# Kernel tuning notes

Hardware: AMD Instinct MI355X
Metric: run time of the kernel (lower is better)

## Reference

```python
import jax, jax.numpy as jnp
import numpy as np

EMBED = 512
HEADS = 8
DIM_HEAD = 64          # embed_dim // 8
LANDMARKS = 256        # embed_dim // 2
PINV_ITERS = 6
RES_K = 33             # nystrom residual_conv_kernel default
SCALE = DIM_HEAD ** -0.5


def layer_norm(x, g, b, eps=1e-5):
    mu = x.mean(-1, keepdims=True)
    var = ((x - mu) ** 2).mean(-1, keepdims=True)
    return (x - mu) / jnp.sqrt(var + eps) * g + b


def moore_penrose_pinv(x, iters=PINV_ITERS):
    # iterative Moore-Penrose pseudo-inverse (lucidrains nystrom-attention)
    ax = jnp.abs(x)
    z = jnp.swapaxes(x, -1, -2) / (ax.sum(-1).max() * ax.sum(-2).max())
    I = jnp.eye(x.shape[-1], dtype=x.dtype)
    for _ in range(iters):
        xz = x @ z
        z = 0.25 * z @ (13. * I - xz @ (15. * I - xz @ (7. * I - xz)))
    return z


def nystrom_attention(x, w_qkv, w_out, b_out, res_k):
    b, n, _ = x.shape
    m = LANDMARKS
    pad = (m - n % m) % m
    xp = jnp.pad(x, ((0, 0), (pad, 0), (0, 0)))  # left-pad like F.pad(..., padding, 0)
    np_ = n + pad
    qkv = (xp @ w_qkv).reshape(b, np_, 3, HEADS, DIM_HEAD)
    q = qkv[:, :, 0].transpose(0, 2, 1, 3) * SCALE   # [b,h,np,dh]
    k = qkv[:, :, 1].transpose(0, 2, 1, 3)
    v = qkv[:, :, 2].transpose(0, 2, 1, 3)
    l = np_ // m
    q_l = q.reshape(b, HEADS, m, l, DIM_HEAD).mean(3)  # [b,h,m,dh]
    k_l = k.reshape(b, HEADS, m, l, DIM_HEAD).mean(3)
    attn1 = jax.nn.softmax(jnp.einsum('bhid,bhjd->bhij', q, k_l), -1)    # [b,h,np,m]
    attn2 = jax.nn.softmax(jnp.einsum('bhid,bhjd->bhij', q_l, k_l), -1)  # [b,h,m,m]
    attn3 = jax.nn.softmax(jnp.einsum('bhid,bhjd->bhij', q_l, k), -1)    # [b,h,m,np]
    out = (attn1 @ moore_penrose_pinv(attn2)) @ (attn3 @ v)              # [b,h,np,dh]
    # depthwise residual conv over the sequence dim, per head (shared across dh)
    v_c = v.transpose(0, 3, 1, 2).reshape(b * DIM_HEAD, HEADS, np_)
    res = jax.lax.conv_general_dilated(
        v_c, res_k[:, None, :], (1,), [(RES_K // 2, RES_K // 2)],
        dimension_numbers=('NCH', 'OIH', 'NCH'), feature_group_count=HEADS)
    out = out + res.reshape(b, DIM_HEAD, HEADS, np_).transpose(0, 2, 3, 1)
    out = out.transpose(0, 2, 1, 3).reshape(b, np_, HEADS * DIM_HEAD)
    out = out @ w_out + b_out
    return out[:, -n:]  # drop left padding


def dwconv2d(x, w, b, k):
    # x: [B,C,H,W], w: [C,1,k,k] depthwise
    y = jax.lax.conv_general_dilated(
        x, w, (1, 1), [(k // 2, k // 2)] * 2,
        dimension_numbers=('NCHW', 'OIHW', 'NCHW'), feature_group_count=x.shape[1])
    return y + b[None, :, None, None]


def ppeg(x, H, W, w7, b7, w5, b5, w3, b3):
    B, _, C = x.shape
    cls_tok, feat = x[:, :1], x[:, 1:]
    f = feat.transpose(0, 2, 1).reshape(B, C, H, W)
    y = f + dwconv2d(f, w7, b7, 7) + dwconv2d(f, w5, b5, 5) + dwconv2d(f, w3, b3, 3)
    y = y.reshape(B, C, H * W).transpose(0, 2, 1)
    return jnp.concatenate([cls_tok, y], axis=1)


def reference(h, w_fc1, b_fc1, cls_token,
              ln1_g, ln1_b, qkv1_w, out1_w, out1_b, res1_k,
              conv7_w, conv7_b, conv5_w, conv5_b, conv3_w, conv3_b,
              ln2_g, ln2_b, qkv2_w, out2_w, out2_b, res2_k,
              lnf_g, lnf_b):
    h = jax.nn.relu(h @ w_fc1 + b_fc1)                 # [B,N,512]
    B, N, C = h.shape
    _H = int(np.ceil(np.sqrt(N)))
    add = _H * _H - N
    h = jnp.concatenate([h, h[:, :add]], axis=1)       # square padding
    h = jnp.concatenate([jnp.broadcast_to(cls_token, (B, 1, C)), h], axis=1)
    h = h + nystrom_attention(layer_norm(h, ln1_g, ln1_b), qkv1_w, out1_w, out1_b, res1_k)
    h = ppeg(h, _H, _H, conv7_w, conv7_b, conv5_w, conv5_b, conv3_w, conv3_b)
    h = h + nystrom_attention(layer_norm(h, ln2_g, ln2_b), qkv2_w, out2_w, out2_b, res2_k)
    return layer_norm(h, lnf_g, lnf_b)[:, 0]           # [B,512]


def setup_inputs() -> dict:
    key = jax.random.key(0)
    ks = jax.random.split(key, 24)
    B, N, IN_DIM = 2, 4096, 1024
    w = lambda k, shape, s=0.02: jax.random.normal(k, shape, jnp.float32) * s
    z = lambda shape: jnp.zeros(shape, jnp.float32)
    o = lambda shape: jnp.ones(shape, jnp.float32)
    return {
        'h': jax.random.normal(ks[0], (B, N, IN_DIM), jnp.float32),
        'w_fc1': w(ks[1], (IN_DIM, EMBED)), 'b_fc1': z((EMBED,)),
        'cls_token': w(ks[2], (1, 1, EMBED)),
        'ln1_g': o((EMBED,)), 'ln1_b': z((EMBED,)),
        'qkv1_w': w(ks[3], (EMBED, 3 * HEADS * DIM_HEAD)),
        'out1_w': w(ks[4], (HEADS * DIM_HEAD, EMBED)), 'out1_b': z((EMBED,)),
        'res1_k': w(ks[5], (HEADS, RES_K), 0.1),
        'conv7_w': w(ks[6], (EMBED, 1, 7, 7), 0.05), 'conv7_b': z((EMBED,)),
        'conv5_w': w(ks[7], (EMBED, 1, 5, 5), 0.05), 'conv5_b': z((EMBED,)),
        'conv3_w': w(ks[8], (EMBED, 1, 3, 3), 0.05), 'conv3_b': z((EMBED,)),
        'ln2_g': o((EMBED,)), 'ln2_b': z((EMBED,)),
        'qkv2_w': w(ks[9], (EMBED, 3 * HEADS * DIM_HEAD)),
        'out2_w': w(ks[10], (HEADS * DIM_HEAD, EMBED)), 'out2_b': z((EMBED,)),
        'res2_k': w(ks[11], (HEADS, RES_K), 0.1),
        'lnf_g': o((EMBED,)), 'lnf_b': z((EMBED,)),
    }
```

## Files before the change

kernel.cpp:

```cpp
#include <hip/hip_runtime.h>
#include <hip/hip_bf16.h>

#define HEADS 8
#define DH 64
#define EMB 512
#define NP 4352
#define NTOK 4097
#define PADF 255
#define LM 256
#define SCALE 0.125f

typedef __attribute__((ext_vector_type(8))) short bf8;
typedef __attribute__((ext_vector_type(4))) float f4;
typedef __attribute__((ext_vector_type(8))) unsigned short us8;
typedef __attribute__((ext_vector_type(4))) unsigned short us4;
typedef unsigned short u16;

__device__ __forceinline__ u16 f2b(float f){
  union { float f; unsigned u; } x; x.f = f;
  unsigned r = x.u + 0x7fffu + ((x.u>>16)&1u);
  return (u16)(r>>16);
}
__device__ __forceinline__ float b2f(u16 h){
  union { unsigned u; float f; } x; x.u = ((unsigned)h)<<16;
  return x.f;
}

__device__ __forceinline__ void gload_lds(const u16* g, u16* l){
  __builtin_amdgcn_global_load_lds((const __attribute__((address_space(1))) void*)g,
                                   (__attribute__((address_space(3))) void*)l, 16, 0, 0);
}

template<int MODE>
__global__ __launch_bounds__(256)
void k_g128(const u16* __restrict__ A, const u16* __restrict__ B,
            float* __restrict__ C, u16* __restrict__ C16,
            int K, int lda, int ldb, int ldc,
            long sAb, long sAh, long sBb, long sBh, long sCb, long sCh, int nh,
            float alpha, const float* __restrict__ bias, int relu, int rowoff,
            int nx, int ksplit)
{
  int z = blockIdx.z;
  const u16* Ab = A + (long)(z/nh)*sAb + (long)(z%nh)*sAh;
  const u16* Bb = B + (long)(z/nh)*sBb + (long)(z%nh)*sBh;
  long cb = (long)(z/nh)*sCb + (long)(z%nh)*sCh;
  int bx = blockIdx.x % nx, kc = blockIdx.x / nx;
  int m0 = blockIdx.y*128, n0 = bx*128;
  int klen = K/ksplit, kbeg = kc*klen, nch = klen/32;
  __shared__ u16 As[2][4096];
  __shared__ u16 Bs[2][4096];
  int tid=threadIdx.x, w=tid>>6, lane=tid&63, q=lane>>4, lr=lane&15;
  int wrow=(w>>1)*64, wcol=(w&1)*64;
  int srow = tid>>2, scol = (tid&3)*8;
  const u16* ga  = Ab + (long)(m0+srow)*lda + kbeg + scol;
  const u16* ga2 = Ab + (long)(m0+64+srow)*lda + kbeg + scol;
  const u16* gb  = Bb + (long)(n0+srow)*ldb + kbeg + scol;
  const u16* gb2 = Bb + (long)(n0+64+srow)*ldb + kbeg + scol;
  int lo = srow*32 + scol;
  f4 acc[4][4] = {};
  auto stage = [&](int r, int c){
    gload_lds(ga  + c*32, &As[r][lo]);
    gload_lds(ga2 + c*32, &As[r][2048+lo]);
    gload_lds(gb  + c*32, &Bs[r][lo]);
    gload_lds(gb2 + c*32, &Bs[r][2048+lo]);
  };
  auto compute = [&](int r){
    bf8 af[4], bfr[4];
    #pragma unroll
    for(int rr=0;rr<4;rr++) af[rr]  = *(const bf8*)&As[r][(wrow + rr*16 + lr)*32 + q*8];
    #pragma unroll
    for(int t=0;t<4;t++) bfr[t] = *(const bf8*)&Bs[r][(wcol + t*16 + lr)*32 + q*8];
    #pragma unroll
    for(int rr=0;rr<4;rr++)
      #pragma unroll
      for(int t=0;t<4;t++)
        acc[rr][t] = __builtin_amdgcn_mfma_f32_16x16x32_bf16(af[rr], bfr[t], acc[rr][t], 0,0,0);
  };
  stage(0,0);
  __syncthreads();
  for(int c=1;c<nch;c++){
    stage(c&1, c);
    compute((c-1)&1);
    __syncthreads();
  }
  compute((nch-1)&1);
  #pragma unroll
  for(int r=0;r<4;r++){
    #pragma unroll
    for(int t=0;t<4;t++){
      #pragma unroll
      for(int e=0;e<4;e++){
        int gm = m0 + wrow + r*16 + q*4 + e;
        int gn = n0 + wcol + t*16 + lr;
        float v = acc[r][t][e]*alpha;
        if(MODE==4){
          if(bias && kc==0) v += bias[gn];
          if(gm>=rowoff) atomicAdd(&C[cb + (long)(gm-rowoff)*ldc + gn], v);
        } else {
          if(bias) v += bias[gn];
          if(relu) v = fmaxf(v,0.f);
          if(MODE==0) C[cb + (long)gm*ldc + gn] = v;
          else if(MODE==2) C16[cb + (long)gm*ldc + gn] = f2b(v);
          else { if(gm>=rowoff) C[cb + (long)(gm-rowoff)*ldc + gn] += v; }
        }
      }
    }
  }
}

template<int MODE>
__global__ __launch_bounds__(256)
void k_g64(const u16* __restrict__ A, const u16* __restrict__ B,
           float* __restrict__ C, u16* __restrict__ C16,
           int K, int lda, int ldb, int ldc,
           long sAb, long sAh, long sBb, long sBh, long sCb, long sCh, int nh,
           float alpha, const float* __restrict__ bias, int rowoff, int moff,
           int nx, int ksplit)
{
  int z = blockIdx.z;
  const u16* Ab = A + (long)(z/nh)*sAb + (long)(z%nh)*sAh;
  const u16* Bb = B + (long)(z/nh)*sBb + (long)(z%nh)*sBh;
  long cb = (long)(z/nh)*sCb + (long)(z%nh)*sCh;
  int bx = blockIdx.x % nx, kc = blockIdx.x / nx;
  int m0 = blockIdx.y*64 + moff, n0 = bx*64;
  int klen = K/ksplit, kbeg = kc*klen, nch = klen/32;
  __shared__ u16 As[2][2048];
  __shared__ u16 Bs[2][2048];
  int tid=threadIdx.x, w=tid>>6, lane=tid&63, q=lane>>4, lr=lane&15;
  int srow = tid>>2, scol = (tid&3)*8;
  const u16* ga = Ab + (long)(m0+srow)*lda + kbeg + scol;
  const u16* gb = Bb + (long)(n0+srow)*ldb + kbeg + scol;
  int lo = srow*32 + scol;
  f4 acc[4] = {};
  auto stage = [&](int r, int c){
    gload_lds(ga + c*32, &As[r][lo]);
    gload_lds(gb + c*32, &Bs[r][lo]);
  };
  auto compute = [&](int r){
    bf8 af = *(const bf8*)&As[r][(w*16 + lr)*32 + q*8];
    #pragma unroll
    for(int t=0;t<4;t++){
      bf8 bfr = *(const bf8*)&Bs[r][(t*16 + lr)*32 + q*8];
      acc[t] = __builtin_amdgcn_mfma_f32_16x16x32_bf16(af, bfr, acc[t], 0,0,0);
    }
  };
  stage(0,0);
  __syncthreads();
  for(int c=1;c<nch;c++){
    stage(c&1, c);
    compute((c-1)&1);
    __syncthreads();
  }
  compute((nch-1)&1);
  #pragma unroll
  for(int t=0;t<4;t++){
    #pragma unroll
    for(int e=0;e<4;e++){
      int gm = m0 + w*16 + q*4 + e;
      int gn = n0 + t*16 + lr;
      float v = acc[t][e]*alpha;
      if(MODE==0) C[cb + (long)gm*ldc + gn] = v;
      else if(MODE==2) C16[cb + (long)gm*ldc + gn] = f2b(v);
      else if(MODE==3) atomicAdd(&C[cb + (long)gm*ldc + gn], v);
      else if(MODE==5){
        v += bias[gn];
        if(gm>=rowoff) C[cb + (long)(gm-rowoff)*ldc + gn] += v;
      }
    }
  }
}

__global__ __launch_bounds__(256)
void k_pg3(const u16* __restrict__ Ah, const u16* __restrict__ Al,
           const u16* __restrict__ Bh, const u16* __restrict__ Bl,
           u16* __restrict__ Oh, u16* __restrict__ Ol, float na, float nd,
           u16* __restrict__ TOh, u16* __restrict__ TOl, float ta, float td)
{
  long zo = (long)blockIdx.z*65536;
  int m0 = blockIdx.y*32, n0 = blockIdx.x*64;
  __shared__ u16 S[2][6144];
  int tid=threadIdx.x, w=tid>>6, lane=tid&63, q=lane>>4, lr=lane&15;
  int t2 = tid & 127;
  const u16* srcA = (tid<128 ? Ah : Al) + zo + (long)(m0 + (t2>>2))*256 + (t2&3)*8;
  const u16* srcBh = Bh + zo + (long)(n0 + (tid>>2))*256 + (tid&3)*8;
  const u16* srcBl = Bl + zo + (long)(n0 + (tid>>2))*256 + (tid&3)*8;
  f4 acc[2] = {};
  auto stage = [&](int r, int c){
    gload_lds(srcA  + c*32, &S[r][tid*8]);
    gload_lds(srcBh + c*32, &S[r][2048 + tid*8]);
    gload_lds(srcBl + c*32, &S[r][4096 + tid*8]);
  };
  int mrow = (w>>1)*16 + lr;
  auto compute = [&](int r){
    bf8 ah = *(const bf8*)&S[r][mrow*32 + q*8];
    bf8 al = *(const bf8*)&S[r][1024 + mrow*32 + q*8];
    #pragma unroll
    for(int t=0;t<2;t++){
      int nrow = (w&1)*32 + t*16 + lr;
      bf8 bh = *(const bf8*)&S[r][2048 + nrow*32 + q*8];
      bf8 bl = *(const bf8*)&S[r][4096 + nrow*32 + q*8];
      acc[t] = __builtin_amdgcn_mfma_f32_16x16x32_bf16(ah, bh, acc[t], 0,0,0);
      acc[t] = __builtin_amdgcn_mfma_f32_16x16x32_bf16(ah, bl, acc[t], 0,0,0);
      acc[t] = __builtin_amdgcn_mfma_f32_16x16x32_bf16(al, bh, acc[t], 0,0,0);
    }
  };
  stage(0,0);
  __syncthreads();
  #pragma unroll
  for(int c=1;c<8;c++){
    stage(c&1, c);
    compute((c-1)&1);
    __syncthreads();
  }
  compute(1);
  #pragma unroll
  for(int t=0;t<2;t++){
    int gn = n0 + (w&1)*32 + t*16 + lr;
    if(Oh){
      #pragma unroll
      for(int r=0;r<4;r++){
        int gm = m0 + (w>>1)*16 + q*4 + r;
        float v = na*acc[t][r] + ((gm==gn)?nd:0.f);
        u16 h = f2b(v);
        long o = zo + (long)gm*256 + gn;
        Oh[o] = h; Ol[o] = f2b(v - b2f(h));
      }
    }
    if(TOh){
      us4 th, tl;
      #pragma unroll
      for(int r=0;r<4;r++){
        int gm = m0 + (w>>1)*16 + q*4 + r;
        float v = ta*acc[t][r] + ((gm==gn)?td:0.f);
        u16 h = f2b(v);
        th[r] = h; tl[r] = f2b(v - b2f(h));
      }
      long o = zo + (long)gn*256 + (m0 + (w>>1)*16 + q*4);
      *(us4*)&TOh[o] = th; *(us4*)&TOl[o] = tl;
    }
  }
}

__global__ __launch_bounds__(256)
void k_pg3b(const u16* __restrict__ Zh, const u16* __restrict__ Zl,
            const u16* __restrict__ Ph, const u16* __restrict__ Pl,
            const u16* __restrict__ Bh, const u16* __restrict__ Bl,
            u16* __restrict__ Ozh, u16* __restrict__ Ozl,
            u16* __restrict__ Oyh, u16* __restrict__ Oyl,
            u16* __restrict__ Tyh, u16* __restrict__ Tyl)
{
  long zo = (long)blockIdx.z*65536;
  int ysel = blockIdx.y>>3;
  int m0 = (blockIdx.y&7)*32, n0 = blockIdx.x*64;
  const u16* Ah = ysel ? Ph : Zh;
  const u16* Al = ysel ? Pl : Zl;
  __shared__ u16 S[2][6144];
  int tid=threadIdx.x, w=tid>>6, lane=tid&63, q=lane>>4, lr=lane&15;
  int t2 = tid & 127;
  const u16* srcA = (tid<128 ? Ah : Al) + zo + (long)(m0 + (t2>>2))*256 + (t2&3)*8;
  const u16* srcBh = Bh + zo + (long)(n0 + (tid>>2))*256 + (tid&3)*8;
  const u16* srcBl = Bl + zo + (long)(n0 + (tid>>2))*256 + (tid&3)*8;
  f4 acc[2] = {};
  auto stage = [&](int r, int c){
    gload_lds(srcA  + c*32, &S[r][tid*8]);
    gload_lds(srcBh + c*32, &S[r][2048 + tid*8]);
    gload_lds(srcBl + c*32, &S[r][4096 + tid*8]);
  };
  int mrow = (w>>1)*16 + lr;
  auto compute = [&](int r){
    bf8 ah = *(const bf8*)&S[r][mrow*32 + q*8];
    bf8 al = *(const bf8*)&S[r][1024 + mrow*32 + q*8];
    #pragma unroll
    for(int t=0;t<2;t++){
      int nrow = (w&1)*32 + t*16 + lr;
      bf8 bh = *(const bf8*)&S[r][2048 + nrow*32 + q*8];
      bf8 bl = *(const bf8*)&S[r][4096 + nrow*32 + q*8];
      acc[t] = __builtin_amdgcn_mfma_f32_16x16x32_bf16(ah, bh, acc[t], 0,0,0);
      acc[t] = __builtin_amdgcn_mfma_f32_16x16x32_bf16(ah, bl, acc[t], 0,0,0);
      acc[t] = __builtin_amdgcn_mfma_f32_16x16x32_bf16(al, bh, acc[t], 0,0,0);
    }
  };
  stage(0,0);
  __syncthreads();
  #pragma unroll
  for(int c=1;c<8;c++){
    stage(c&1, c);
    compute((c-1)&1);
    __syncthreads();
  }
  compute(1);
  #pragma unroll
  for(int t=0;t<2;t++){
    int gn = n0 + (w&1)*32 + t*16 + lr;
    if(!ysel){
      #pragma unroll
      for(int r=0;r<4;r++){
        int gm = m0 + (w>>1)*16 + q*4 + r;
        float v = 0.25f*acc[t][r];
        u16 h = f2b(v);
        long o = zo + (long)gm*256 + gn;
        Ozh[o] = h; Ozl[o] = f2b(v - b2f(h));
      }
    } else {
      us4 th, tl;
      #pragma unroll
      for(int r=0;r<4;r++){
        int gm = m0 + (w>>1)*16 + q*4 + r;
        float v = 0.25f*acc[t][r];
        u16 h = f2b(v);
        long o = zo + (long)gm*256 + gn;
        Oyh[o] = h; Oyl[o] = f2b(v - b2f(h));
        float tv = -v + ((gm==gn)?7.f:0.f);
        u16 h2 = f2b(tv);
        th[r] = h2; tl[r] = f2b(tv - b2f(h2));
      }
      long o = zo + (long)gn*256 + (m0 + (w>>1)*16 + q*4);
      *(us4*)&Tyh[o] = th; *(us4*)&Tyl[o] = tl;
    }
  }
}

__global__ __launch_bounds__(256)
void k_att3(const u16* __restrict__ qkv16, const u16* __restrict__ ql,
            const u16* __restrict__ vT, float* __restrict__ partO,
            float* __restrict__ pm, float* __restrict__ pl)
{
  int kc = blockIdx.x, jt = blockIdx.y, z = blockIdx.z;
  int b = z>>3, h = z&7;
  __shared__ u16 SQ[64*64];
  __shared__ u16 SK[2][64*64];
  __shared__ u16 SV[2][64*64];
  __shared__ u16 SP[64*64];
  int tid=threadIdx.x, w=tid>>6, lane=tid&63, q=lane>>4, lr=lane&15;
  const u16* kb = qkv16 + (long)b*NP*1536 + 512 + h*64;
  const u16* vb = vT + (long)z*64*NP;
  int t00 = kc*256;
  {
    const u16* qb = ql + (long)z*16384 + jt*64*64;
    #pragma unroll
    for(int p=0;p<2;p++){
      int idx = tid + p*256; int row = idx>>3; int js = ((idx&7)^(row&7))<<3;
      gload_lds(qb + row*64 + js, &SQ[idx*8]);
    }
  }
  auto stageKV = [&](int r, int i){
    int t0 = t00 + i*64;
    #pragma unroll
    for(int p=0;p<2;p++){
      int idx = tid + p*256; int row = idx>>3; int js = ((idx&7)^(row&7))<<3;
      gload_lds(kb + (long)(t0+row)*1536 + js, &SK[r][idx*8]);
      gload_lds(vb + (long)row*NP + t0 + js, &SV[r][idx*8]);
    }
  };
  stageKV(0,0);
  __syncthreads();
  int ar = w*16+lr;
  bf8 af0 = *(const bf8*)&SQ[ar*64 + ((q^(ar&7))<<3)];
  bf8 af1 = *(const bf8*)&SQ[ar*64 + (((q|4)^(ar&7))<<3)];
  f4 o[4] = {};
  float m[4] = {-3e38f,-3e38f,-3e38f,-3e38f};
  float l[4] = {0.f,0.f,0.f,0.f};
  for(int i=0;i<4;i++){
    int cur = i&1;
    if(i<3) stageKV(cur^1, i+1);
    f4 s[4] = {};
    #pragma unroll
    for(int t=0;t<4;t++){
      int br = t*16+lr;
      bf8 b0 = *(const bf8*)&SK[cur][br*64 + ((q^(br&7))<<3)];
      bf8 b1 = *(const bf8*)&SK[cur][br*64 + (((q|4)^(br&7))<<3)];
      s[t] = __builtin_amdgcn_mfma_f32_16x16x32_bf16(af0, b0, s[t], 0,0,0);
      s[t] = __builtin_amdgcn_mfma_f32_16x16x32_bf16(af1, b1, s[t], 0,0,0);
    }
    float tm[4];
    #pragma unroll
    for(int e=0;e<4;e++) tm[e] = fmaxf(fmaxf(s[0][e],s[1][e]), fmaxf(s[2][e],s[3][e]));
    #pragma unroll
    for(int sh=1; sh<16; sh<<=1)
      #pragma unroll
      for(int e=0;e<4;e++) tm[e] = fmaxf(tm[e], __shfl_xor(tm[e], sh));
    float rs[4];
    #pragma unroll
    for(int e=0;e<4;e++){
      float mn = fmaxf(m[e], tm[e]);
      float sc = expf(m[e]-mn);
      m[e] = mn;
      l[e] *= sc;
      rs[e] = 0.f;
      o[0][e]*=sc; o[1][e]*=sc; o[2][e]*=sc; o[3][e]*=sc;
    }
    #pragma unroll
    for(int t=0;t<4;t++)
      #pragma unroll
      for(int e=0;e<4;e++){
        float p = expf(s[t][e]-m[e]);
        rs[e] += p;
        int prow = w*16+q*4+e, pcol = t*16+lr;
        SP[prow*64 + (((pcol>>3)^(prow&7))<<3) + (pcol&7)] = f2b(p);
      }
    #pragma unroll
    for(int sh=1; sh<16; sh<<=1)
      #pragma unroll
      for(int e=0;e<4;e++) rs[e] += __shfl_xor(rs[e], sh);
    #pragma unroll
    for(int e=0;e<4;e++) l[e] += rs[e];
    int pr = w*16+lr;
    #pragma unroll
    for(int ks=0;ks<2;ks++){
      bf8 pa = *(const bf8*)&SP[pr*64 + (((ks*4+q)^(pr&7))<<3)];
      #pragma unroll
      for(int t2=0;t2<4;t2++){
        int rr = t2*16+lr;
        bf8 vv = *(const bf8*)&SV[cur][rr*64 + (((ks*4+q)^(rr&7))<<3)];
        o[t2] = __builtin_amdgcn_mfma_f32_16x16x32_bf16(pa, vv, o[t2], 0,0,0);
      }
    }
    __syncthreads();
  }
  long pb = (long)(z*17+kc)*256 + jt*64 + w*16;
  #pragma unroll
  for(int e=0;e<4;e++){
    int jg = q*4+e;
    #pragma unroll
    for(int t2=0;t2<4;t2++)
      partO[(pb + jg)*64 + t2*16 + lr] = o[t2][e];
    if(lr==0){ pm[pb + jg] = m[e]; pl[pb + jg] = l[e]; }
  }
}

__global__ __launch_bounds__(128)
void k_mrg3(const float* __restrict__ partO, const float* __restrict__ pm,
            const float* __restrict__ pl, u16* __restrict__ avbT16)
{
  int jq = blockIdx.x, z = blockIdx.y, tid = threadIdx.x;
  int j0 = jq*16;
  __shared__ float wk[16][17];
  __shared__ u16 T[16][72];
  if(tid < 16){
    int j = j0 + tid;
    float mm[17];
    float M = -3e38f;
    #pragma unroll
    for(int kc=0;kc<17;kc++){ mm[kc]=pm[(z*17+kc)*256 + j]; M=fmaxf(M,mm[kc]); }
    float s = 0.f;
    #pragma unroll
    for(int kc=0;kc<17;kc++){ float e=expf(mm[kc]-M); wk[tid][kc]=e; s+=e*pl[(z*17+kc)*256 + j]; }
    float inv = 1.f/s;
    #pragma unroll
    for(int kc=0;kc<17;kc++) wk[tid][kc]*=inv;
  }
  __syncthreads();
  float acc[8];
  #pragma unroll
  for(int p=0;p<8;p++) acc[p]=0.f;
  for(int kc=0;kc<17;kc++){
    long base = ((long)(z*17+kc)*256 + j0)*64;
    #pragma unroll
    for(int p=0;p<8;p++){
      int idx = tid + p*128;
      acc[p] += wk[idx>>6][kc]*partO[base + idx];
    }
  }
  #pragma unroll
  for(int p=0;p<8;p++){ int idx = tid + p*128; T[idx>>6][idx&63] = f2b(acc[p]); }
  __syncthreads();
  int d = tid>>1, jh = (tid&1)*8;
  us8 vv;
  #pragma unroll
  for(int u=0;u<8;u++) vv[u] = T[jh+u][d];
  *(us8*)&avbT16[(long)(z*64+d)*256 + j0 + jh] = vv;
}

__global__ __launch_bounds__(256)
void k_att1(const u16* __restrict__ qkv16, const u16* __restrict__ kl,
            const u16* __restrict__ zavT, float* __restrict__ Qc)
{
  int z = blockIdx.y, b = z>>3, h = z&7;
  int m0 = blockIdx.x*64;
  __shared__ u16 SQ[64*64];
  __shared__ u16 SKL[256*64];
  __shared__ u16 SZV[64*256];
  int tid=threadIdx.x, w=tid>>6, lane=tid&63, q=lane>>4, lr=lane&15;
  {
    const u16* qb = qkv16 + (long)b*NP*1536 + h*64;
    #pragma unroll
    for(int p=0;p<2;p++){
      int idx = tid + p*256; int row = idx>>3; int js = ((idx&7)^(row&7))<<3;
      gload_lds(qb + (long)(m0+row)*1536 + js, &SQ[idx*8]);
    }
    const u16* kb = kl + (long)z*16384;
    #pragma unroll
    for(int p=0;p<8;p++){
      int idx = tid + p*256; int row = idx>>3; int js = ((idx&7)^(row&7))<<3;
      gload_lds(kb + row*64 + js, &SKL[idx*8]);
    }
    const u16* zb = zavT + (long)z*16384;
    #pragma unroll
    for(int p=0;p<8;p++){
      int idx = tid + p*256; int row = idx>>5; int cs = ((idx&31)^(row&7))<<3;
      gload_lds(zb + row*256 + cs, &SZV[idx*8]);
    }
  }
  __syncthreads();
  f4 acc[16] = {};
  {
    int ar = w*16+lr;
    bf8 af0 = *(const bf8*)&SQ[ar*64 + ((q^(ar&7))<<3)];
    bf8 af1 = *(const bf8*)&SQ[ar*64 + (((q|4)^(ar&7))<<3)];
    #pragma unroll
    for(int t=0;t<16;t++){
      int br = t*16+lr;
      bf8 b0 = *(const bf8*)&SKL[br*64 + ((q^(br&7))<<3)];
      bf8 b1 = *(const bf8*)&SKL[br*64 + (((q|4)^(br&7))<<3)];
      acc[t] = __builtin_amdgcn_mfma_f32_16x16x32_bf16(af0, b0, acc[t], 0,0,0);
      acc[t] = __builtin_amdgcn_mfma_f32_16x16x32_bf16(af1, b1, acc[t], 0,0,0);
    }
  }
  float mx[4] = {-1e30f,-1e30f,-1e30f,-1e30f};
  #pragma unroll
  for(int t=0;t<16;t++)
    #pragma unroll
    for(int e=0;e<4;e++) mx[e] = fmaxf(mx[e], acc[t][e]*SCALE);
  #pragma unroll
  for(int s=1;s<16;s<<=1)
    #pragma unroll
    for(int e=0;e<4;e++) mx[e] = fmaxf(mx[e], __shfl_xor(mx[e], s));
  float sm[4] = {0.f,0.f,0.f,0.f};
  #pragma unroll
  for(int t=0;t<16;t++)
    #pragma unroll
    for(int e=0;e<4;e++){ float p = expf(acc[t][e]*SCALE - mx[e]); acc[t][e]=p; sm[e]+=p; }
  #pragma unroll
  for(int s=1;s<16;s<<=1)
    #pragma unroll
    for(int e=0;e<4;e++) sm[e] += __shfl_xor(sm[e], s);
  float inv[4];
  #pragma unroll
  for(int e=0;e<4;e++) inv[e] = 1.f/sm[e];
  __syncthreads();
  u16* PS = SKL;
  #pragma unroll
  for(int t=0;t<16;t++)
    #pragma unroll
    for(int e=0;e<4;e++){
      int prow = w*16 + q*4 + e, pcol = t*16 + lr;
      PS[prow*256 + (((pcol>>3)^(prow&7))<<3) + (pcol&7)] = f2b(acc[t][e]*inv[e]);
    }
  __syncthreads();
  f4 acc2[4] = {};
  int pr = w*16+lr;
  #pragma unroll
  for(int ks=0;ks<8;ks++){
    bf8 af = *(const bf8*)&PS[pr*256 + (((ks*4+q)^(pr&7))<<3)];
    #pragma unroll
    for(int t=0;t<4;t++){
      int rr = t*16+lr;
      bf8 bf_ = *(const bf8*)&SZV[rr*256 + (((ks*4+q)^(rr&7))<<3)];
      acc2[t] = __builtin_amdgcn_mfma_f32_16x16x32_bf16(af, bf_, acc2[t], 0,0,0);
    }
  }
  #pragma unroll
  for(int t=0;t<4;t++)
    #pragma unroll
    for(int r=0;r<4;r++){
      int gm = m0 + w*16 + q*4 + r;
      int gd = t*16 + lr;
      Qc[((long)b*NP + gm)*512 + h*64 + gd] = acc2[t][r];
    }
}

__global__ __launch_bounds__(256)
void k_smw32(float* __restrict__ X){
  long row = (long)blockIdx.x*4 + (threadIdx.x>>6);
  int lane = threadIdx.x & 63;
  float* p = X + row*256;
  float4 v = *(float4*)&p[lane*4];
  float m = fmaxf(fmaxf(v.x,v.y),fmaxf(v.z,v.w));
  for(int s=32;s;s>>=1) m = fmaxf(m, __shfl_xor(m, s));
  float e0=expf(v.x-m), e1=expf(v.y-m), e2=expf(v.z-m), e3=expf(v.w-m);
  float sum = e0+e1+e2+e3;
  for(int s=32;s;s>>=1) sum += __shfl_xor(sum, s);
  float inv = 1.f/sum;
  float4 o = {e0*inv, e1*inv, e2*inv, e3*inv};
  *(float4*)&p[lane*4] = o;
}

__global__ void k_wT(const float* __restrict__ in, u16* __restrict__ out, int K, int N){
  int n0=blockIdx.x*32, k0=blockIdx.y*32, tid=threadIdx.x;
  __shared__ float T[32][33];
  int lr=tid&31, lc=tid>>5;
  #pragma unroll
  for(int p=0;p<4;p++) T[lc+8*p][lr] = in[(long)(k0+lc+8*p)*N + n0+lr];
  __syncthreads();
  #pragma unroll
  for(int p=0;p<4;p++) out[(long)(n0+lc+8*p)*K + k0+lr] = f2b(T[lr][lc+8*p]);
}

__global__ __launch_bounds__(256)
void k_vT(const u16* __restrict__ qkv16, u16* __restrict__ vT){
  int t0=blockIdx.x*64, h=blockIdx.y, b=blockIdx.z, tid=threadIdx.x;
  __shared__ u16 T[64][72];
  const u16* src = qkv16 + (long)b*NP*1536 + 1024 + h*64;
  for(int s=0;s<2;s++){
    int idx=tid+s*256; int row=idx>>3, c8=(idx&7)*8;
    *(us8*)&T[row][c8] = *(const us8*)&src[(long)(t0+row)*1536 + c8];
  }
  __syncthreads();
  u16* dst = vT + ((long)(b*8+h)*64)*NP;
  int d = tid>>2, j0=(tid&3)*16;
  us8 v0,v1;
  #pragma unroll
  for(int jj=0;jj<8;jj++){ v0[jj]=T[j0+jj][d]; v1[jj]=T[j0+8+jj][d]; }
  *(us8*)&dst[(long)d*NP + t0 + j0]     = v0;
  *(us8*)&dst[(long)d*NP + t0 + j0 + 8] = v1;
}

__global__ void k_cvt16(const float* __restrict__ in, u16* __restrict__ out, long n){
  long i = (long)blockIdx.x*256 + threadIdx.x;
  if(i<n) out[i] = f2b(in[i]);
}

__global__ void k_cls(const float* __restrict__ cls, float* __restrict__ seq){
  int b = blockIdx.x;
  seq[(long)b*NTOK*EMB + threadIdx.x] = cls[threadIdx.x];
}

__global__ void k_ln_pad(const float* __restrict__ seq, u16* __restrict__ xp,
                         const float* __restrict__ g, const float* __restrict__ bb){
  int b = blockIdx.y, i = blockIdx.x, tid = threadIdx.x;
  u16* out = xp + ((long)b*NP + i)*EMB;
  if(i < PADF){ out[tid]=0; out[tid+256]=0; return; }
  const float* x = seq + ((long)b*NTOK + (i-PADF))*EMB;
  float v0 = x[tid], v1 = x[tid+256];
  __shared__ float red[256];
  red[tid]=v0+v1; __syncthreads();
  for(int s=128;s>0;s>>=1){ if(tid<s) red[tid]+=red[tid+s]; __syncthreads(); }
  float mu = red[0]*(1.0f/512.0f); __syncthreads();
  float d0=v0-mu, d1=v1-mu;
  red[tid]=d0*d0+d1*d1; __syncthreads();
  for(int s=128;s>0;s>>=1){ if(tid<s) red[tid]+=red[tid+s]; __syncthreads(); }
  float rstd = rsqrtf(red[0]*(1.0f/512.0f) + 1e-5f);
  out[tid]     = f2b(d0*rstd*g[tid]     + bb[tid]);
  out[tid+256] = f2b(d1*rstd*g[tid+256] + bb[tid+256]);
}

__global__ void k_landmarks(const u16* __restrict__ qkv, u16* __restrict__ q_l, u16* __restrict__ k_l){
  int j = blockIdx.x*4 + (threadIdx.x>>6), h = blockIdx.y, b = blockIdx.z, d = threadIdx.x&63;
  const u16* base = qkv + (long)b*NP*1536 + h*64 + d;
  float sq=0.f, sk=0.f;
  for(int l=0;l<17;l++){
    long row = (long)(j*17+l)*1536;
    sq += b2f(base[row]);
    sk += b2f(base[row+512]);
  }
  long o = (((long)b*HEADS + h)*LM + j)*DH + d;
  q_l[o] = f2b(sq * (SCALE/17.0f));
  k_l[o] = f2b(sk * (1.0f/17.0f));
}

__global__ void k_pinv_norm(const float* __restrict__ A2, float* __restrict__ rmax, float* __restrict__ cmax){
  int z = blockIdx.x, tid = threadIdx.x;
  const float* X = A2 + (long)z*65536;
  float rs=0.f, cs=0.f;
  for(int j=0;j<256;j++){ rs += fabsf(X[tid*256+j]); cs += fabsf(X[j*256+tid]); }
  __shared__ float r1[256], r2[256];
  r1[tid]=rs; r2[tid]=cs; __syncthreads();
  for(int s=128;s>0;s>>=1){ if(tid<s){ r1[tid]=fmaxf(r1[tid],r1[tid+s]); r2[tid]=fmaxf(r2[tid],r2[tid+s]); } __syncthreads(); }
  if(tid==0){ rmax[z]=r1[0]; cmax[z]=r2[0]; }
}

__global__ void k_pair_init(const float* __restrict__ att2,
    const float* __restrict__ rmax, const float* __restrict__ cmax,
    u16* __restrict__ Xh, u16* __restrict__ Xl,
    u16* __restrict__ Zh, u16* __restrict__ Zl,
    u16* __restrict__ Zth, u16* __restrict__ Ztl)
{
  long zo = (long)blockIdx.z*65536;
  int i0 = blockIdx.y*64, j0 = blockIdx.x*64;
  float rm=0.f, cm=0.f;
  for(int t=0;t<16;t++){ rm=fmaxf(rm,rmax[t]); cm=fmaxf(cm,cmax[t]); }
  float inv = 1.0f/(rm*cm);
  __shared__ float T[64][68];
  int tid = threadIdx.x;
  int li = tid>>2, jc = (tid&3)*16;
  #pragma unroll
  for(int u=0;u<4;u++){
    float4 v = *(const float4*)&att2[zo + (long)(i0+li)*256 + j0 + jc + u*4];
    T[li][jc+u*4]=v.x; T[li][jc+u*4+1]=v.y; T[li][jc+u*4+2]=v.z; T[li][jc+u*4+3]=v.w;
    long o = zo + (long)(i0+li)*256 + j0 + jc + u*4;
    float vv[4] = {v.x,v.y,v.z,v.w};
    us4 xh, xl, zth, ztl;
    #pragma unroll
    for(int c=0;c<4;c++){
      u16 h = f2b(vv[c]); xh[c]=h; xl[c]=f2b(vv[c]-b2f(h));
      float zt = vv[c]*inv;
      u16 h2 = f2b(zt); zth[c]=h2; ztl[c]=f2b(zt-b2f(h2));
    }
    *(us4*)&Xh[o]=xh; *(us4*)&Xl[o]=xl; *(us4*)&Zth[o]=zth; *(us4*)&Ztl[o]=ztl;
  }
  __syncthreads();
  int lj = tid>>2, ic = (tid&3)*16;
  #pragma unroll
  for(int r=0;r<16;r++){
    float x = T[ic+r][lj]*inv;
    u16 h = f2b(x);
    long o = zo + (long)(j0+lj)*256 + i0 + ic + r;
    Zh[o]=h; Zl[o]=f2b(x-b2f(h));
  }
}

__global__ __launch_bounds__(256)
void k_rconv(const u16* __restrict__ qkv16, const float* __restrict__ resk,
             const float* __restrict__ Qin, u16* __restrict__ Qo16){
  int t0 = blockIdx.x*64, h = blockIdx.y, b = blockIdx.z;
  __shared__ float V[96*64];
  const u16* vb = qkv16 + (long)b*NP*1536 + 1024 + h*64;
  int tid = threadIdx.x;
  #pragma unroll
  for(int s=0;s<3;s++){
    int idx = tid + s*256;
    int row = idx>>3, c8 = (idx&7)*8;
    int p = t0 - 16 + row;
    if(p>=0 && p<NP){
      us8 v = *(const us8*)&vb[(long)p*1536 + c8];
      #pragma unroll
      for(int jj=0;jj<8;jj++) V[row*64+c8+jj] = b2f(v[jj]);
    } else {
      #pragma unroll
      for(int jj=0;jj<8;jj++) V[row*64+c8+jj] = 0.f;
    }
  }
  __syncthreads();
  int d = tid&63, lt = (tid>>6)*16;
  float acc[16] = {};
  #pragma unroll
  for(int s=0;s<48;s++){
    float val = V[(lt+s)*64 + d];
    #pragma unroll
    for(int j=0;j<16;j++){
      int tap = s - j;
      if(tap>=0 && tap<33) acc[j] += resk[h*33+tap]*val;
    }
  }
  #pragma unroll
  for(int j=0;j<16;j++){
    long idx = ((long)b*NP + t0 + lt + j)*EMB + h*64 + d;
    Qo16[idx] = f2b(Qin[idx] + acc[j]);
  }
}

__global__ __launch_bounds__(256)
void k_ppeg(const float* __restrict__ seq, float* __restrict__ out,
    const float* __restrict__ w7,const float* __restrict__ b7,
    const float* __restrict__ w5,const float* __restrict__ b5,
    const float* __restrict__ w3,const float* __restrict__ b3){
  int b = blockIdx.z, cg = blockIdx.y;
  int rp = blockIdx.x>>1, xs = blockIdx.x&1;
  int ch0 = cg*64;
  __shared__ float s7[64*49], s5[64*25], s3[64*9], sbias[64];
  int tid = threadIdx.x;
  for(int i=tid;i<64*49;i+=256) s7[i] = w7[ch0*49+i];
  for(int i=tid;i<64*25;i+=256) s5[i] = w5[ch0*25+i];
  for(int i=tid;i<64*9;i+=256)  s3[i] = w3[ch0*9+i];
  if(tid<64) sbias[tid] = b7[ch0+tid]+b5[ch0+tid]+b3[ch0+tid];
  if(cg==0 && blockIdx.x==0){
    out[(long)b*NTOK*EMB + tid]       = seq[(long)b*NTOK*EMB + tid];
    out[(long)b*NTOK*EMB + 256 + tid] = seq[(long)b*NTOK*EMB + 256 + tid];
  }
  __syncthreads();
  int c = tid & 63;
  int y = rp*4 + (tid>>6);
  const float* sbase = seq + (long)b*NTOK*EMB + EMB + (ch0 + c);
  float* obase = out + (long)b*NTOK*EMB + EMB + (ch0 + c);
  const float* W7 = &s7[c*49];
  const float* W5 = &s5[c*25];
  const float* W3 = &s3[c*9];
  float bsum = sbias[c];
  for(int xc=0;xc<4;xc++){
    int xb = xs*32 + xc*8;
    float acc[8];
    #pragma unroll
    for(int j=0;j<8;j++) acc[j] = sbase[(long)(y*64+xb+j)*EMB] + bsum;
    #pragma unroll
    for(int dy=-3;dy<=3;dy++){
      int yy = y+dy;
      if(yy<0||yy>=64) continue;
      float v[14];
      #pragma unroll
      for(int u=0;u<14;u++){
        int xx = xb + u - 3;
        v[u] = (xx>=0 && xx<64) ? sbase[(long)(yy*64+xx)*EMB] : 0.f;
      }
      #pragma unroll
      for(int dx=-3;dx<=3;dx++){
        float wsum = W7[(dy+3)*7+(dx+3)];
        if(dy>=-2&&dy<=2&&dx>=-2&&dx<=2) wsum += W5[(dy+2)*5+(dx+2)];
        if(dy>=-1&&dy<=1&&dx>=-1&&dx<=1) wsum += W3[(dy+1)*3+(dx+1)];
        #pragma unroll
        for(int j=0;j<8;j++) acc[j] += v[j+dx+3]*wsum;
      }
    }
    #pragma unroll
    for(int j=0;j<8;j++) obase[(long)(y*64+xb+j)*EMB] = acc[j];
  }
}

__global__ void k_final_ln(const float* __restrict__ seq, const float* __restrict__ g,
                           const float* __restrict__ bb, float* __restrict__ out){
  int b = blockIdx.x, tid = threadIdx.x;
  const float* x = seq + (long)b*NTOK*EMB;
  float v0 = x[tid], v1 = x[tid+256];
  __shared__ float red[256];
  red[tid]=v0+v1; __syncthreads();
  for(int s=128;s>0;s>>=1){ if(tid<s) red[tid]+=red[tid+s]; __syncthreads(); }
  float mu = red[0]*(1.0f/512.0f); __syncthreads();
  float d0=v0-mu, d1=v1-mu;
  red[tid]=d0*d0+d1*d1; __syncthreads();
  for(int s=128;s>0;s>>=1){ if(tid<s) red[tid]+=red[tid+s]; __syncthreads(); }
  float rstd = rsqrtf(red[0]*(1.0f/512.0f) + 1e-5f);
  out[b*512+tid]     = d0*rstd*g[tid]     + bb[tid];
  out[b*512+tid+256] = d1*rstd*g[tid+256] + bb[tid+256];
}

extern "C" void kernel_launch(void* const* d_in, const int* in_sizes, int n_in,
                              void* d_out, int out_size, void* d_ws, size_t ws_size,
                              hipStream_t stream) {
  const float* in[24];
  for(int i=0;i<24;i++) in[i] = (const float*)d_in[i];

  float* W = (float*)d_ws;
  size_t off = 0;
  float* seqA = W+off; off += 4195328;
  float* seqB = W+off; off += 4195328;
  float* att2 = W+off; off += 1048576;
  float* Qc   = W+off; off += 4456448;
  float* partO= W+off; off += 17825792;
  float* pm   = W+off; off += 69632;
  float* pl   = W+off; off += 69632;
  u16* xpb    = (u16*)(W+off); off += 2228224;
  u16* qkvb16 = (u16*)(W+off); off += 6684672;
  u16* vT16   = (u16*)(W+off); off += 2228224;
  u16* q_l16  = (u16*)(W+off); off += 131072;
  u16* k_l16  = (u16*)(W+off); off += 131072;
  u16* avbT16 = (u16*)(W+off); off += 131072;
  u16* zavT16 = (u16*)(W+off); off += 131072;
  u16* Qc16   = (u16*)(W+off); off += 2228224;
  u16* qkvwT1 = (u16*)(W+off); off += 393216;
  u16* qkvwT2 = (u16*)(W+off); off += 393216;
  u16* outwT1 = (u16*)(W+off); off += 131072;
  u16* outwT2 = (u16*)(W+off); off += 131072;
  u16* pairs  = (u16*)(W+off); off += 9437184;
  float* rmax = W+off; off += 16;
  float* cmax = W+off; off += 16;
  if (ws_size < off*sizeof(float)) return;

  u16* h16   = pairs;
  u16* wfc1T = pairs + 8388608;

  const long PB = 1048576;
  u16 *Xh=pairs,        *Xl=pairs+PB;
  u16 *Z0h=pairs+2*PB,  *Z0l=pairs+3*PB;
  u16 *Z0th=pairs+4*PB, *Z0tl=pairs+5*PB;
  u16 *Z1h=pairs+6*PB,  *Z1l=pairs+7*PB;
  u16 *P0h=pairs+8*PB,  *P0l=pairs+9*PB;
  u16 *P1h=pairs+10*PB, *P1l=pairs+11*PB;
  u16 *Tth=pairs+12*PB, *Ttl=pairs+13*PB;
  u16 *Uth=pairs+14*PB, *Utl=pairs+15*PB;
  u16 *Vth=pairs+16*PB, *Vtl=pairs+17*PB;

  k_cvt16<<<32768,256,0,stream>>>(in[0], h16, 8388608L);
  k_wT<<<dim3(16,32),256,0,stream>>>(in[1],  wfc1T, 1024, 512);
  k_wT<<<dim3(48,16),256,0,stream>>>(in[6],  qkvwT1, 512, 1536);
  k_wT<<<dim3(48,16),256,0,stream>>>(in[18], qkvwT2, 512, 1536);
  k_wT<<<dim3(16,16),256,0,stream>>>(in[7],  outwT1, 512, 512);
  k_wT<<<dim3(16,16),256,0,stream>>>(in[19], outwT2, 512, 512);

  k_g128<0><<<dim3(4,32,2),256,0,stream>>>(h16, wfc1T, seqA+EMB, nullptr,
      1024, 1024,1024,512, 4194304L,0, 0,0, (long)NTOK*EMB,0, 1, 1.0f, in[2], 1, 0, 4, 1);
  k_cls<<<2,512,0,stream>>>(in[3], seqA);

  auto attention = [&](float* seq, const float* lng,const float* lnb,
                       const u16* qkvwT, const u16* outwT, const float* outb, const float* resk){
    k_ln_pad<<<dim3(NP,2),256,0,stream>>>(seq, xpb, lng, lnb);
    k_g128<2><<<dim3(12,34,2),256,0,stream>>>(xpb, qkvwT, nullptr, qkvb16,
        512, 512,512,1536, (long)NP*512,0, 0,0, (long)NP*1536,0, 1, 1.0f, nullptr, 0, 0, 12, 1);
    k_landmarks<<<dim3(64,HEADS,2),256,0,stream>>>(qkvb16, q_l16, k_l16);
    k_vT<<<dim3(68,8,2),256,0,stream>>>(qkvb16, vT16);
    k_g128<0><<<dim3(2,2,16),256,0,stream>>>(q_l16, k_l16, att2, nullptr,
        64, 64,64,256, 0,16384, 0,16384, 0,65536, 16, 1.0f, nullptr, 0, 0, 2, 1);
    k_smw32<<<1024,256,0,stream>>>(att2);
    k_pinv_norm<<<16,256,0,stream>>>(att2, rmax, cmax);
    k_pair_init<<<dim3(4,4,16),256,0,stream>>>(att2, rmax, cmax, Xh,Xl, Z0h,Z0l, Z0th,Z0tl);
    dim3 pgrid(4,8,16);
    k_pg3<<<pgrid,256,0,stream>>>(Xh,Xl, Z0th,Z0tl, P0h,P0l,1.0f,0.f, Tth,Ttl,-1.0f,7.f);
    for(int it=0; it<6; it++){
      u16 *Zh_=(it&1)?Z1h:Z0h, *Zl_=(it&1)?Z1l:Z0l;
      u16 *Nh_=(it&1)?Z0h:Z1h, *Nl_=(it&1)?Z0l:Z1l;
      u16 *Pch=(it&1)?P1h:P0h, *Pcl=(it&1)?P1l:P0l;
      u16 *Pnh=(it&1)?P0h:P1h, *Pnl=(it&1)?P0l:P1l;
      k_pg3<<<pgrid,256,0,stream>>>(Pch,Pcl, Tth,Ttl, nullptr,nullptr,0.f,0.f, Uth,Utl,-1.0f,15.f);
      k_pg3<<<pgrid,256,0,stream>>>(Pch,Pcl, Uth,Utl, nullptr,nullptr,0.f,0.f, Vth,Vtl,-1.0f,13.f);
      if(it<5) k_pg3b<<<dim3(4,16,16),256,0,stream>>>(Zh_,Zl_, Pch,Pcl, Vth,Vtl,
                                                      Nh_,Nl_, Pnh,Pnl, Tth,Ttl);
      else     k_pg3<<<pgrid,256,0,stream>>>(Zh_,Zl_, Vth,Vtl, Nh_,Nl_,0.25f,0.f,
                                             nullptr,nullptr,0.f,0.f);
    }
    k_att3<<<dim3(17,4,16),256,0,stream>>>(qkvb16, q_l16, vT16, partO, pm, pl);
    k_mrg3<<<dim3(16,16),128,0,stream>>>(partO, pm, pl, avbT16);
    k_g64<2><<<dim3(4,1,16),256,0,stream>>>(avbT16, Z0h, nullptr, zavT16,
        256, 256,256,256, 0,16384L, 0,65536L, 0,16384L, 16, 1.0f, nullptr, 0, 0, 4, 1);
    k_att1<<<dim3(68,16),256,0,stream>>>(qkvb16, k_l16, zavT16, Qc);
    k_rconv<<<dim3(68,8,2),256,0,stream>>>(qkvb16, resk, Qc, Qc16);
    k_g64<5><<<dim3(8,65,2),256,0,stream>>>(Qc16, outwT, seq, nullptr,
        512, 512,512,512, (long)NP*512,0, 0,0, (long)NTOK*EMB,0, 1, 1.0f, outb, PADF, 192, 8, 1);
  };

  attention(seqA, in[4], in[5], qkvwT1, outwT1, in[8], in[9]);
  k_ppeg<<<dim3(32,8,2),256,0,stream>>>(seqA, seqB, in[10],in[11],in[12],in[13],in[14],in[15]);
  attention(seqB, in[16], in[17], qkvwT2, outwT2, in[20], in[21]);
  k_final_ln<<<2,256,0,stream>>>(seqB, in[22], in[23], (float*)d_out);
}
```

Baseline: 917.5 us.

## Prefetch two K-chunks ahead with explicit vmcnt waits in GEMM pipelines

Restructures the double-buffered main loops of four GEMM kernels so two chunks are in flight. Each iteration waits only for the older chunk's global-to-LDS loads via partial s_waitcnt vmcnt, then computes, then refills the freed buffer with chunk c+2. This is meant to hide global load latency behind MFMA work instead of draining all loads at every __syncthreads. Correctness now depends on the hand-set vmcnt counts matching the number of loads each stage issues, and every iteration has two barriers.

```diff
diff --git a/kernel.cpp b/kernel.cpp
--- a/kernel.cpp
+++ b/kernel.cpp
@@ -30,6 +30,10 @@
   __builtin_amdgcn_global_load_lds((const __attribute__((address_space(1))) void*)g,
                                    (__attribute__((address_space(3))) void*)l, 16, 0, 0);
 }
+
+#define WAITCNT(N) asm volatile("s_waitcnt vmcnt(" #N ")" ::: "memory")
+#define SCHED_FENCE() __builtin_amdgcn_sched_barrier(0)
+#define BARRIER() __builtin_amdgcn_s_barrier()
 
 template<int MODE>
 __global__ __launch_bounds__(256)
@@ -77,13 +81,17 @@
         acc[rr][t] = __builtin_amdgcn_mfma_f32_16x16x32_bf16(af[rr], bfr[t], acc[rr][t], 0,0,0);
   };
   stage(0,0);
-  __syncthreads();
-  for(int c=1;c<nch;c++){
-    stage(c&1, c);
-    compute((c-1)&1);
-    __syncthreads();
-  }
-  compute((nch-1)&1);
+  stage(1,1);
+  for(int c=0;c<nch;c++){
+    if(c+1<nch) WAITCNT(4); else WAITCNT(0);
+    SCHED_FENCE();
+    BARRIER();
+    compute(c&1);
+    SCHED_FENCE();
+    BARRIER();
+    SCHED_FENCE();
+    if(c+2<nch) stage(c&1, c+2);
+  }
   #pragma unroll
   for(int r=0;r<4;r++){
     #pragma unroll
@@ -145,13 +153,17 @@
     }
   };
   stage(0,0);
-  __syncthreads();
-  for(int c=1;c<nch;c++){
-    stage(c&1, c);
-    compute((c-1)&1);
-    __syncthreads();
-  }
-  compute((nch-1)&1);
+  stage(1,1);
+  for(int c=0;c<nch;c++){
+    if(c+1<nch) WAITCNT(2); else WAITCNT(0);
+    SCHED_FENCE();
+    BARRIER();
+    compute(c&1);
+    SCHED_FENCE();
+    BARRIER();
+    SCHED_FENCE();
+    if(c+2<nch) stage(c&1, c+2);
+  }
   #pragma unroll
   for(int t=0;t<4;t++){
     #pragma unroll
@@ -205,14 +217,17 @@
     }
   };
   stage(0,0);
-  __syncthreads();
-  #pragma unroll
-  for(int c=1;c<8;c++){
-    stage(c&1, c);
-    compute((c-1)&1);
-    __syncthreads();
-  }
-  compute(1);
+  stage(1,1);
+  for(int c=0;c<8;c++){
+    if(c<7) WAITCNT(3); else WAITCNT(0);
+    SCHED_FENCE();
+    BARRIER();
+    compute(c&1);
+    SCHED_FENCE();
+    BARRIER();
+    SCHED_FENCE();
+    if(c+2<8) stage(c&1, c+2);
+  }
   #pragma unroll
   for(int t=0;t<2;t++){
     int gn = n0 + (w&1)*32 + t*16 + lr;
@@ -281,14 +296,17 @@
     }
   };
   stage(0,0);
-  __syncthreads();
-  #pragma unroll
-  for(int c=1;c<8;c++){
-    stage(c&1, c);
-    compute((c-1)&1);
-    __syncthreads();
-  }
-  compute(1);
+  stage(1,1);
+  for(int c=0;c<8;c++){
+    if(c<7) WAITCNT(3); else WAITCNT(0);
+    SCHED_FENCE();
+    BARRIER();
+    compute(c&1);
+    SCHED_FENCE();
+    BARRIER();
+    SCHED_FENCE();
+    if(c+2<8) stage(c&1, c+2);
+  }
   #pragma unroll
   for(int t=0;t<2;t++){
     int gn = n0 + (w&1)*32 + t*16 + lr;
```

New measurement: 879.7 us. 1.04x faster.
